# Kernel optimization log

Measured on AMD Instinct MI355X. Metric: run time of the kernel, lower is better.

The kernel has to match this reference:

```python
import jax, jax.numpy as jnp
import numpy as np

PATCH = 16
LOSS_WEIGHT = 1.0


def setup_inputs() -> dict:
    key = jax.random.key(0)
    cls_score = jax.random.normal(key, (8, 19, 512, 512), dtype=jnp.float32)
    return {"cls_score": cls_score}


def reference(cls_score):
    # Faithful to NuclearLoss(patch_size=16, use_softmax=True, inverse=False,
    # reduction='mean').
    N, C, H, W = cls_score.shape
    p = PATCH
    ph, pw = H // p, W // p
    logits = jax.nn.softmax(cls_score, axis=1)  # softmax over channel dim
    # patchify: (N,C,H,W) -> (N*L, p*p, C) with L = ph*pw
    x = logits.reshape(N, C, ph, p, pw, p)
    x = jnp.einsum('nchpwq->nhwpqc', x)
    patches = x.reshape(N * ph * pw, p * p, C)  # (B, p^2, C)
    # Original: mats = sqrt(bmm(P^T, P)) elementwise, loss = -sum(trace(mat)).
    # Only the diagonal of P^T P is needed: diag_k = sum_i P[i,k]^2.
    diag = jnp.sum(patches * patches, axis=1)          # (B, C)
    loss = -jnp.sum(jnp.sqrt(diag))
    loss = loss / patches.shape[0]                      # reduction='mean'
    return LOSS_WEIGHT * loss
```

## Files before the change

### kernel.cpp

```cpp
#include <hip/hip_runtime.h>
#include <math.h>


#define NIMG 8
#define CCH  19
#define HH   512
#define WW   512
#define CHST (HH * WW)

template <int CTRL>
__device__ __forceinline__ float dpp_add(float x) {
    int t = __builtin_amdgcn_update_dpp(0, __float_as_int(x), CTRL, 0xF, 0xF, true);
    return x + __int_as_float(t);
}

__global__ __launch_bounds__(256, 4) void nuclear_loss_kernel(
    const float* __restrict__ in, float* __restrict__ out) {
    __shared__ float psum[4 * 4 * CCH];
    __shared__ float total;

    const int tid  = threadIdx.x;
    const int b    = blockIdx.x;
    const int n    = b >> 8;
    const int rem  = b & 255;
    const int prow = rem >> 3;
    const int creg = rem & 7;
    const int w    = tid >> 6;
    const int l    = tid & 63;
    const int p    = l >> 4;
    const int r    = (l >> 2) & 3;
    const int cq   = l & 3;

    if (tid == 0) total = 0.0f;

    const int row = (prow << 4) + (w << 2) + r;
    const int col = (creg << 6) + (p << 4) + (cq << 2);
    const float* bp = in + (size_t)n * (size_t)(CCH * CHST)
                         + (size_t)row * WW + col;

    float4 v[CCH];
#pragma unroll
    for (int c = 0; c < CCH; ++c)
        v[c] = *reinterpret_cast<const float4*>(bp + (size_t)c * CHST);

    float sx = 0.f, sy = 0.f, sz = 0.f, sw = 0.f;
#pragma unroll
    for (int c = 0; c < CCH; ++c) {
        v[c].x = __expf(v[c].x); sx += v[c].x;
        v[c].y = __expf(v[c].y); sy += v[c].y;
        v[c].z = __expf(v[c].z); sz += v[c].z;
        v[c].w = __expf(v[c].w); sw += v[c].w;
    }
    const float ix = __builtin_amdgcn_rcpf(sx);
    const float iy = __builtin_amdgcn_rcpf(sy);
    const float iz = __builtin_amdgcn_rcpf(sz);
    const float iw = __builtin_amdgcn_rcpf(sw);

    const bool lead = ((l & 15) == 12);

#pragma unroll
    for (int c = 0; c < CCH; ++c) {
        const float tx = v[c].x * ix;
        const float ty = v[c].y * iy;
        const float tz = v[c].z * iz;
        const float tw = v[c].w * iw;
        float x = tx * tx;
        x = fmaf(ty, ty, x);
        x = fmaf(tz, tz, x);
        x = fmaf(tw, tw, x);
        x = dpp_add<0xB1>(x);
        x = dpp_add<0x4E>(x);
        x = dpp_add<0x114>(x);
        x = dpp_add<0x118>(x);
        if (lead)
            psum[(w << 2 | p) * CCH + c] = x;
    }
    __syncthreads();

    if (tid < 128) {
        float acc = 0.0f;
        if (tid < 4 * CCH) {
            const float s4 = psum[tid] + psum[76 + tid]
                           + psum[152 + tid] + psum[228 + tid];
            acc = sqrtf(s4);
        }
        acc += __shfl_down(acc, 32, 64);
        acc += __shfl_down(acc, 16, 64);
        acc += __shfl_down(acc, 8, 64);
        acc += __shfl_down(acc, 4, 64);
        acc += __shfl_down(acc, 2, 64);
        acc += __shfl_down(acc, 1, 64);
        if (l == 0) atomicAdd(&total, acc);
    }
    __syncthreads();
    if (tid == 0) atomicAdd(out, total * (-1.0f / 8192.0f));
}

extern "C" void kernel_launch(void* const* d_in, const int* in_sizes, int n_in,
                              void* d_out, int out_size, void* d_ws, size_t ws_size,
                              hipStream_t stream) {
    const float* in = (const float*)d_in[0];
    float* out = (float*)d_out;
    hipMemsetAsync(out, 0, sizeof(float), stream);
    nuclear_loss_kernel<<<2048, 256, 0, stream>>>(in, out);
}
```

Before: 220.1 us.

## Stage channel loads through LDS with async global_load_lds ring buffer

Replaces the 19 direct float4 global loads per thread with asynchronous global-to-LDS loads into an 8-slot per-wave ring. Each slot uses an XOR-swizzled address, and explicit vmcnt/lgkmcnt waits interleave issuing and consuming. The aim is to pipeline memory traffic and free registers while loads are in flight. In exchange it adds 32 KB of LDS per block and limits outstanding loads to 8, which can reduce memory-level parallelism.

```diff
diff --git a/kernel.cpp b/kernel.cpp
--- a/kernel.cpp
+++ b/kernel.cpp
@@ -14,8 +14,12 @@
     return x + __int_as_float(t);
 }
 
+typedef __attribute__((address_space(1))) const unsigned int gbuf_t;
+typedef __attribute__((address_space(3))) unsigned int lbuf_t;
+
 __global__ __launch_bounds__(256, 4) void nuclear_loss_kernel(
     const float* __restrict__ in, float* __restrict__ out) {
+    __shared__ __align__(16) float stage[4][8][256];
     __shared__ float psum[4 * 4 * CCH];
     __shared__ float total;
 
@@ -26,22 +30,53 @@
     const int prow = rem >> 3;
     const int creg = rem & 7;
     const int w    = tid >> 6;
-    const int l    = tid & 63;
-    const int p    = l >> 4;
-    const int r    = (l >> 2) & 3;
-    const int cq   = l & 3;
+    const int g    = tid & 63;
+    const int p    = g >> 4;
+    const int r    = (g >> 2) & 3;
+    const int cq   = g & 3;
 
     if (tid == 0) total = 0.0f;
 
-    const int row = (prow << 4) + (w << 2) + r;
-    const int col = (creg << 6) + (p << 4) + (cq << 2);
-    const float* bp = in + (size_t)n * (size_t)(CCH * CHST)
-                         + (size_t)row * WW + col;
+    const float* wbase = in + (size_t)n * (size_t)(CCH * CHST)
+                            + (size_t)((prow << 4) + (w << 2)) * WW
+                            + (creg << 6);
+
+#define ISSUE(c, s)                                                            \
+    do {                                                                       \
+        const int h_  = g ^ (((c) & 15) << 2);                                 \
+        const int off = (((h_ >> 2) & 3) * WW) + (((h_ >> 4) & 3) << 4)        \
+                        + ((h_ & 3) << 2);                                     \
+        __builtin_amdgcn_global_load_lds(                                      \
+            (gbuf_t*)(wbase + (size_t)(c) * CHST + off),                       \
+            (lbuf_t*)&stage[w][s][0], 16, 0, 0);                               \
+    } while (0)
+
+#define READC(c, s)                                                            \
+    v[c] = *reinterpret_cast<const float4*>(                                   \
+        &stage[w][s][(g ^ (((c) & 15) << 2)) << 2])
+
+#define WAITVM(N) asm volatile("s_waitcnt vmcnt(" #N ")" ::: "memory")
+#define DRAINLGKM() asm volatile("s_waitcnt lgkmcnt(0)" ::: "memory")
 
     float4 v[CCH];
-#pragma unroll
-    for (int c = 0; c < CCH; ++c)
-        v[c] = *reinterpret_cast<const float4*>(bp + (size_t)c * CHST);
+    ISSUE(0, 0); ISSUE(1, 1); ISSUE(2, 2); ISSUE(3, 3);
+    ISSUE(4, 4); ISSUE(5, 5); ISSUE(6, 6); ISSUE(7, 7);
+    WAITVM(4);
+    READC(0, 0); READC(1, 1); READC(2, 2); READC(3, 3);
+    DRAINLGKM();
+    ISSUE(8, 0); ISSUE(9, 1); ISSUE(10, 2); ISSUE(11, 3);
+    WAITVM(4);
+    READC(4, 4); READC(5, 5); READC(6, 6); READC(7, 7);
+    DRAINLGKM();
+    ISSUE(12, 4); ISSUE(13, 5); ISSUE(14, 6); ISSUE(15, 7);
+    WAITVM(4);
+    READC(8, 0); READC(9, 1); READC(10, 2); READC(11, 3);
+    DRAINLGKM();
+    ISSUE(16, 0); ISSUE(17, 1); ISSUE(18, 2);
+    WAITVM(3);
+    READC(12, 4); READC(13, 5); READC(14, 6); READC(15, 7);
+    WAITVM(0);
+    READC(16, 0); READC(17, 1); READC(18, 2);
 
     float sx = 0.f, sy = 0.f, sz = 0.f, sw = 0.f;
 #pragma unroll
@@ -56,7 +91,7 @@
     const float iz = __builtin_amdgcn_rcpf(sz);
     const float iw = __builtin_amdgcn_rcpf(sw);
 
-    const bool lead = ((l & 15) == 12);
+    const bool lead = ((g & 15) == 12);
 
 #pragma unroll
     for (int c = 0; c < CCH; ++c) {
@@ -90,7 +125,7 @@
         acc += __shfl_down(acc, 4, 64);
         acc += __shfl_down(acc, 2, 64);
         acc += __shfl_down(acc, 1, 64);
-        if (l == 0) atomicAdd(&total, acc);
+        if (g == 0) atomicAdd(&total, acc);
     }
     __syncthreads();
     if (tid == 0) atomicAdd(out, total * (-1.0f / 8192.0f));
```

Result: no change. 221.1 us (+0.5%).

## Split into row-strip pass with global patch-sum atomics and a sqrt-reduce pass

Applied to the files above, without the earlier changes.

Each block now processes two full image rows (512 columns) instead of a 16x64 tile, so each wave reads long contiguous row segments per channel. Per-patch partial sums of squares are accumulated through shared-memory atomics and then global atomics into a workspace buffer. A second kernel applies sqrt and reduces across all patches. This adds a memset, a second launch, and many global float atomics in exchange for better coalescing of the input reads.

```diff
diff --git a/kernel.cpp b/kernel.cpp
--- a/kernel.cpp
+++ b/kernel.cpp
@@ -7,6 +7,8 @@
 #define HH   512
 #define WW   512
 #define CHST (HH * WW)
+#define NPATCH 8192
+#define PSUM_ELEMS (NPATCH * CCH)
 
 template <int CTRL>
 __device__ __forceinline__ float dpp_add(float x) {
@@ -14,29 +16,24 @@
     return x + __int_as_float(t);
 }
 
-__global__ __launch_bounds__(256, 4) void nuclear_loss_kernel(
-    const float* __restrict__ in, float* __restrict__ out) {
-    __shared__ float psum[4 * 4 * CCH];
-    __shared__ float total;
+__global__ __launch_bounds__(256, 4) void nuclear_pass1(
+    const float* __restrict__ in, float* __restrict__ psum_g) {
+    __shared__ float psum[32 * CCH];
 
-    const int tid  = threadIdx.x;
-    const int b    = blockIdx.x;
-    const int n    = b >> 8;
-    const int rem  = b & 255;
-    const int prow = rem >> 3;
-    const int creg = rem & 7;
-    const int w    = tid >> 6;
-    const int l    = tid & 63;
-    const int p    = l >> 4;
-    const int r    = (l >> 2) & 3;
-    const int cq   = l & 3;
+    const int tid   = threadIdx.x;
+    const int b     = blockIdx.x;
+    const int n     = b >> 8;
+    const int r2    = b & 255;
+    const int colg  = tid & 127;
+    const int rhalf = tid >> 7;
+    const int pc    = colg >> 2;
 
-    if (tid == 0) total = 0.0f;
+    for (int i = tid; i < 32 * CCH; i += 256) psum[i] = 0.0f;
+    __syncthreads();
 
-    const int row = (prow << 4) + (w << 2) + r;
-    const int col = (creg << 6) + (p << 4) + (cq << 2);
+    const int row = (r2 << 1) + rhalf;
     const float* bp = in + (size_t)n * (size_t)(CCH * CHST)
-                         + (size_t)row * WW + col;
+                         + (size_t)row * WW + (colg << 2);
 
     float4 v[CCH];
 #pragma unroll
@@ -56,7 +53,7 @@
     const float iz = __builtin_amdgcn_rcpf(sz);
     const float iw = __builtin_amdgcn_rcpf(sw);
 
-    const bool lead = ((l & 15) == 12);
+    const bool lead = ((tid & 3) == 3);
 
 #pragma unroll
     for (int c = 0; c < CCH; ++c) {
@@ -70,30 +67,35 @@
         x = fmaf(tw, tw, x);
         x = dpp_add<0xB1>(x);
         x = dpp_add<0x4E>(x);
-        x = dpp_add<0x114>(x);
-        x = dpp_add<0x118>(x);
         if (lead)
-            psum[(w << 2 | p) * CCH + c] = x;
+            atomicAdd(&psum[pc * CCH + c], x);
     }
     __syncthreads();
 
-    if (tid < 128) {
-        float acc = 0.0f;
-        if (tid < 4 * CCH) {
-            const float s4 = psum[tid] + psum[76 + tid]
-                           + psum[152 + tid] + psum[228 + tid];
-            acc = sqrtf(s4);
-        }
-        acc += __shfl_down(acc, 32, 64);
-        acc += __shfl_down(acc, 16, 64);
-        acc += __shfl_down(acc, 8, 64);
-        acc += __shfl_down(acc, 4, 64);
-        acc += __shfl_down(acc, 2, 64);
-        acc += __shfl_down(acc, 1, 64);
-        if (l == 0) atomicAdd(&total, acc);
-    }
+    const int pr = r2 >> 3;
+    float* dst = psum_g + (size_t)((n << 5) + pr) * (32 * CCH);
+    for (int i = tid; i < 32 * CCH; i += 256)
+        atomicAdd(&dst[i], psum[i]);
+}
+
+__global__ __launch_bounds__(256, 8) void nuclear_pass2(
+    const float* __restrict__ psum_g, float* __restrict__ out) {
+    __shared__ float wsum[4];
+    float acc = 0.0f;
+    for (int i = blockIdx.x * 256 + threadIdx.x; i < PSUM_ELEMS;
+         i += gridDim.x * 256)
+        acc += sqrtf(psum_g[i]);
+    acc += __shfl_down(acc, 32, 64);
+    acc += __shfl_down(acc, 16, 64);
+    acc += __shfl_down(acc, 8, 64);
+    acc += __shfl_down(acc, 4, 64);
+    acc += __shfl_down(acc, 2, 64);
+    acc += __shfl_down(acc, 1, 64);
+    if ((threadIdx.x & 63) == 0) wsum[threadIdx.x >> 6] = acc;
     __syncthreads();
-    if (tid == 0) atomicAdd(out, total * (-1.0f / 8192.0f));
+    if (threadIdx.x == 0)
+        atomicAdd(out, (wsum[0] + wsum[1] + wsum[2] + wsum[3])
+                           * (-1.0f / 8192.0f));
 }
 
 extern "C" void kernel_launch(void* const* d_in, const int* in_sizes, int n_in,
@@ -101,6 +103,9 @@
                               hipStream_t stream) {
     const float* in = (const float*)d_in[0];
     float* out = (float*)d_out;
+    float* psum_g = (float*)d_ws;
     hipMemsetAsync(out, 0, sizeof(float), stream);
-    nuclear_loss_kernel<<<2048, 256, 0, stream>>>(in, out);
+    hipMemsetAsync(psum_g, 0, PSUM_ELEMS * sizeof(float), stream);
+    nuclear_pass1<<<2048, 256, 0, stream>>>(in, psum_g);
+    nuclear_pass2<<<128, 256, 0, stream>>>(psum_g, out);
 }
```

New measurement: 224.1 us. No clear change (+1.8%).

## Process pixels in float2 pairs over two iterations to cut registers

Applied to the files above, without the earlier changes.

Each thread now loads two adjacent pixels as float2 for two patches in sequence, instead of four pixels as float4 held all at once. This roughly halves the live register array, and the launch bound is raised to target 8 blocks per SM. The per-channel reduction gains an extra DPP row-broadcast step over 32 lanes. The trade-off is narrower 8-byte loads, less memory-level parallelism per thread, and more DPP instructions per pixel.

```diff
diff --git a/kernel.cpp b/kernel.cpp
--- a/kernel.cpp
+++ b/kernel.cpp
@@ -8,13 +8,13 @@
 #define WW   512
 #define CHST (HH * WW)
 
-template <int CTRL>
+template <int CTRL, int RMASK = 0xF>
 __device__ __forceinline__ float dpp_add(float x) {
-    int t = __builtin_amdgcn_update_dpp(0, __float_as_int(x), CTRL, 0xF, 0xF, true);
+    int t = __builtin_amdgcn_update_dpp(0, __float_as_int(x), CTRL, RMASK, 0xF, true);
     return x + __int_as_float(t);
 }
 
-__global__ __launch_bounds__(256, 4) void nuclear_loss_kernel(
+__global__ __launch_bounds__(256, 8) void nuclear_loss_kernel(
     const float* __restrict__ in, float* __restrict__ out) {
     __shared__ float psum[4 * 4 * CCH];
     __shared__ float total;
@@ -26,54 +26,50 @@
     const int prow = rem >> 3;
     const int creg = rem & 7;
     const int w    = tid >> 6;
-    const int l    = tid & 63;
-    const int p    = l >> 4;
-    const int r    = (l >> 2) & 3;
-    const int cq   = l & 3;
+    const int g    = tid & 63;
+    const int ph   = g >> 5;
+    const int r    = (g >> 3) & 3;
+    const int cp   = g & 7;
 
     if (tid == 0) total = 0.0f;
 
     const int row = (prow << 4) + (w << 2) + r;
-    const int col = (creg << 6) + (p << 4) + (cq << 2);
-    const float* bp = in + (size_t)n * (size_t)(CCH * CHST)
-                         + (size_t)row * WW + col;
-
-    float4 v[CCH];
-#pragma unroll
-    for (int c = 0; c < CCH; ++c)
-        v[c] = *reinterpret_cast<const float4*>(bp + (size_t)c * CHST);
-
-    float sx = 0.f, sy = 0.f, sz = 0.f, sw = 0.f;
-#pragma unroll
-    for (int c = 0; c < CCH; ++c) {
-        v[c].x = __expf(v[c].x); sx += v[c].x;
-        v[c].y = __expf(v[c].y); sy += v[c].y;
-        v[c].z = __expf(v[c].z); sz += v[c].z;
-        v[c].w = __expf(v[c].w); sw += v[c].w;
-    }
-    const float ix = __builtin_amdgcn_rcpf(sx);
-    const float iy = __builtin_amdgcn_rcpf(sy);
-    const float iz = __builtin_amdgcn_rcpf(sz);
-    const float iw = __builtin_amdgcn_rcpf(sw);
-
-    const bool lead = ((l & 15) == 12);
+    const float* rowbase = in + (size_t)n * (size_t)(CCH * CHST)
+                              + (size_t)row * WW + (creg << 6) + (cp << 1);
 
 #pragma unroll
-    for (int c = 0; c < CCH; ++c) {
-        const float tx = v[c].x * ix;
-        const float ty = v[c].y * iy;
-        const float tz = v[c].z * iz;
-        const float tw = v[c].w * iw;
-        float x = tx * tx;
-        x = fmaf(ty, ty, x);
-        x = fmaf(tz, tz, x);
-        x = fmaf(tw, tw, x);
-        x = dpp_add<0xB1>(x);
-        x = dpp_add<0x4E>(x);
-        x = dpp_add<0x114>(x);
-        x = dpp_add<0x118>(x);
-        if (lead)
-            psum[(w << 2 | p) * CCH + c] = x;
+    for (int it = 0; it < 2; ++it) {
+        const int p = (it << 1) | ph;
+        const float* bp = rowbase + (p << 4);
+
+        float2 e[CCH];
+#pragma unroll
+        for (int c = 0; c < CCH; ++c)
+            e[c] = *reinterpret_cast<const float2*>(bp + (size_t)c * CHST);
+
+        float s0 = 0.f, s1 = 0.f;
+#pragma unroll
+        for (int c = 0; c < CCH; ++c) {
+            e[c].x = __expf(e[c].x); s0 += e[c].x;
+            e[c].y = __expf(e[c].y); s1 += e[c].y;
+        }
+        const float i0 = __builtin_amdgcn_rcpf(s0);
+        const float i1 = __builtin_amdgcn_rcpf(s1);
+
+#pragma unroll
+        for (int c = 0; c < CCH; ++c) {
+            const float t0 = e[c].x * i0;
+            const float t1 = e[c].y * i1;
+            float x = t0 * t0;
+            x = fmaf(t1, t1, x);
+            x = dpp_add<0xB1>(x);
+            x = dpp_add<0x4E>(x);
+            x = dpp_add<0x114>(x);
+            x = dpp_add<0x118>(x);
+            x = dpp_add<0x142, 0xa>(x);
+            if ((g & 31) == 31)
+                psum[(w << 2 | p) * CCH + c] = x;
+        }
     }
     __syncthreads();
 
@@ -90,7 +86,7 @@
         acc += __shfl_down(acc, 4, 64);
         acc += __shfl_down(acc, 2, 64);
         acc += __shfl_down(acc, 1, 64);
-        if (l == 0) atomicAdd(&total, acc);
+        if (g == 0) atomicAdd(&total, acc);
     }
     __syncthreads();
     if (tid == 0) atomicAdd(out, total * (-1.0f / 8192.0f));
```

Result: no change. 221.0 us (+0.4%).
